# Kernel optimization log

Hardware: AMD Instinct MI355X
Metric: run time of the kernel (lower is better)

The kernel has to match this reference:

```python
import jax, jax.numpy as jnp
import numpy as np

D = 1024        # d_hidden
DE = 512        # d_expert (routed)
E = 8           # n_routed_experts
TOP_K = 2
DS = DE * 2     # shared expert width = d_expert * n_shared_experts


def setup_inputs() -> dict:
    key = jax.random.key(0)
    ks = jax.random.split(key, 8)
    s = 1.0 / np.sqrt(D)
    return {
        "x": jax.random.normal(ks[0], (2, 1024, D), dtype=jnp.float32),
        "W_g": jax.random.normal(ks[1], (D, E), dtype=jnp.float32) * s,
        "Wg_e": jax.random.normal(ks[2], (E, D, DE), dtype=jnp.float32) * s,
        "Wu_e": jax.random.normal(ks[3], (E, D, DE), dtype=jnp.float32) * s,
        "Wd_e": jax.random.normal(ks[4], (E, DE, D), dtype=jnp.float32) * (1.0 / np.sqrt(DE)),
        "Wg_s": jax.random.normal(ks[5], (D, DS), dtype=jnp.float32) * s,
        "Wu_s": jax.random.normal(ks[6], (D, DS), dtype=jnp.float32) * s,
        "Wd_s": jax.random.normal(ks[7], (DS, D), dtype=jnp.float32) * (1.0 / np.sqrt(DS)),
    }


def _moe(x, W_g, Wg_e, Wu_e, Wd_e, Wg_s, Wu_s, Wd_s):
    B, T, Dm = x.shape
    N = B * T
    xf = x.reshape(N, Dm)

    # shared expert (SwiGLU)
    shared = (jax.nn.silu(xf @ Wg_s) * (xf @ Wu_s)) @ Wd_s  # [N, D]

    # gating: softmax then top-k (set membership identical to torch sorted=False)
    probs = jax.nn.softmax(xf @ W_g, axis=-1)               # [N, E]
    topk_vals, topk_ids = jax.lax.top_k(probs, TOP_K)       # [N, K]

    # combine weights c[n, e] = sum of topk_vals where routed to expert e
    # (equivalent to the original gather -> weighted scatter_add combine)
    c = jnp.zeros((N, E), dtype=x.dtype)
    c = c.at[jnp.arange(N)[:, None], topk_ids].add(topk_vals)

    # dense per-expert SwiGLU, weighted-combined (same math as gather/scatter loop)
    gate = jax.nn.silu(jnp.einsum('nd,edh->neh', xf, Wg_e))
    up = jnp.einsum('nd,edh->neh', xf, Wu_e)
    routed = jnp.einsum('neh,ne,ehd->nd', gate * up, c, Wd_e)  # [N, D]

    return (shared + routed).reshape(B, T, Dm)


def reference(x, W_g, Wg_e, Wu_e, Wd_e, Wg_s, Wu_s, Wd_s):
    return _moe(x, W_g, Wg_e, Wu_e, Wd_e, Wg_s, Wu_s, Wd_s)
```

## Files before the change

### kernel.cpp

```cpp
#include <hip/hip_runtime.h>
#include <hip/hip_bf16.h>

#define NTOK 2048
#define DIM  1024
#define DEXP 512
#define NEXP 8
#define DSH  1024
#define KH   5120
#define MAXROWS 5120

typedef __hip_bfloat16 bf16;
typedef __attribute__((ext_vector_type(8))) short bf16x8;
typedef __attribute__((ext_vector_type(4))) float floatx4;

__device__ __forceinline__ void gl_lds16(const bf16* g, bf16* l) {
    __builtin_amdgcn_global_load_lds(
        (const __attribute__((address_space(1))) void*)g,
        (__attribute__((address_space(3))) void*)l, 16, 0, 0);
}

__device__ __forceinline__ float b2f(short s) {
    union { float f; unsigned u; } v;
    v.u = ((unsigned)(unsigned short)s) << 16;
    return v.f;
}

struct B4 { bf16 a, b, c, d; };

__global__ __launch_bounds__(256) void gate_logits(const float* __restrict__ x,
                                                   const float* __restrict__ Wg,
                                                   bf16* __restrict__ Xb,
                                                   int2* __restrict__ te,
                                                   float2* __restrict__ tp) {
    int t = blockIdx.x * 4 + (threadIdx.x >> 6);
    int lane = threadIdx.x & 63;
    const float* xr = x + (long)t * DIM;
    bf16* xo = Xb + (long)t * DIM;
    float acc[NEXP] = {0.f, 0.f, 0.f, 0.f, 0.f, 0.f, 0.f, 0.f};
#pragma unroll
    for (int i = 0; i < 4; i++) {
        int d = lane * 4 + i * 256;
        float4 xv = *(const float4*)(xr + d);
        B4 o{__float2bfloat16(xv.x), __float2bfloat16(xv.y),
             __float2bfloat16(xv.z), __float2bfloat16(xv.w)};
        *(B4*)(xo + d) = o;
#pragma unroll
        for (int j = 0; j < 4; j++) {
            float xs = (j == 0) ? xv.x : (j == 1) ? xv.y : (j == 2) ? xv.z : xv.w;
            float4 w0 = *(const float4*)(Wg + (d + j) * NEXP);
            float4 w1 = *(const float4*)(Wg + (d + j) * NEXP + 4);
            acc[0] += xs * w0.x; acc[1] += xs * w0.y; acc[2] += xs * w0.z; acc[3] += xs * w0.w;
            acc[4] += xs * w1.x; acc[5] += xs * w1.y; acc[6] += xs * w1.z; acc[7] += xs * w1.w;
        }
    }
#pragma unroll
    for (int e = 0; e < NEXP; e++)
#pragma unroll
        for (int off = 32; off; off >>= 1)
            acc[e] += __shfl_xor(acc[e], off);
    if (lane == 0) {
        float m = acc[0];
#pragma unroll
        for (int e = 1; e < NEXP; e++) m = fmaxf(m, acc[e]);
        float p[NEXP], s = 0.f;
#pragma unroll
        for (int e = 0; e < NEXP; e++) { p[e] = expf(acc[e] - m); s += p[e]; }
        float inv = 1.f / s;
#pragma unroll
        for (int e = 0; e < NEXP; e++) p[e] *= inv;
        int i1 = 0;
#pragma unroll
        for (int e = 1; e < NEXP; e++) if (p[e] > p[i1]) i1 = e;
        int i2 = (i1 == 0) ? 1 : 0;
#pragma unroll
        for (int e = 0; e < NEXP; e++) if (e != i1 && p[e] > p[i2]) i2 = e;
        te[t] = make_int2(i1, i2);
        tp[t] = make_float2(p[i1], p[i2]);
    }
}

__global__ __launch_bounds__(512) void assign_kernel(const int2* __restrict__ te,
                                                     const float2* __restrict__ tp,
                                                     int* __restrict__ counts,
                                                     int* __restrict__ offs,
                                                     int* __restrict__ tok_list,
                                                     float* __restrict__ cw,
                                                     int* __restrict__ s1a,
                                                     int* __restrict__ s2a) {
    __shared__ int cnt[NEXP];
    const int e = threadIdx.x >> 6;
    const int lane = threadIdx.x & 63;
    int base = 0;
    for (int t0 = 0; t0 < NTOK; t0 += 64) {
        int t = t0 + lane;
        int2 ee = te[t];
        bool m1 = (ee.x == e), m2 = (ee.y == e);
        bool mt = m1 || m2;
        unsigned long long mask = __ballot(mt);
        int pre = __popcll(mask & ((1ull << lane) - 1ull));
        if (mt) {
            int slot = base + pre;
            tok_list[e * NTOK + slot] = t;
            float2 pp = tp[t];
            cw[e * NTOK + slot] = m1 ? pp.x : pp.y;
            if (m1) s1a[t] = slot; else s2a[t] = slot;
        }
        base += __popcll(mask);
    }
    if (lane == 0) cnt[e] = base;
    __syncthreads();
    if (threadIdx.x == 0) {
        int o = 0;
#pragma unroll
        for (int i = 0; i < NEXP; i++) {
            counts[i] = cnt[i];
            offs[i] = o;
            o += (cnt[i] + 127) & ~127;
        }
    }
}

__global__ __launch_bounds__(256) void pack_weights(
        const float* __restrict__ Wg_s, const float* __restrict__ Wu_s,
        const float* __restrict__ Wg_e, const float* __restrict__ Wu_e,
        const float* __restrict__ Wd_s, const float* __restrict__ Wd_e,
        bf16* __restrict__ Bg, bf16* __restrict__ Bu, bf16* __restrict__ Bd) {
    __shared__ float t[32][36];
    int b = blockIdx.x;
    const float* src; bf16* dst; int C; long dstStride, dstBase; int tilesX;
    if (b < 1024)       { src = Wg_s; dst = Bg; C = 1024; dstStride = 1024; dstBase = 0; tilesX = 32; }
    else if (b < 2048)  { b -= 1024; src = Wu_s; dst = Bu; C = 1024; dstStride = 1024; dstBase = 0; tilesX = 32; }
    else if (b < 6144)  { b -= 2048; int z = b >> 9; b &= 511;
                          src = Wg_e + (long)z * DIM * DEXP; dst = Bg; C = 512;
                          dstStride = 1024; dstBase = (long)(DSH + z * DEXP) * 1024; tilesX = 16; }
    else if (b < 10240) { b -= 6144; int z = b >> 9; b &= 511;
                          src = Wu_e + (long)z * DIM * DEXP; dst = Bu; C = 512;
                          dstStride = 1024; dstBase = (long)(DSH + z * DEXP) * 1024; tilesX = 16; }
    else if (b < 11264) { b -= 10240; src = Wd_s; dst = Bd; C = 1024; dstStride = KH; dstBase = 0; tilesX = 32; }
    else                { b -= 11264; int z = b >> 9; b &= 511;
                          src = Wd_e + (long)z * DEXP * DIM; dst = Bd; C = 1024;
                          dstStride = KH; dstBase = DSH + (long)z * DEXP; tilesX = 32; }
    int tileX = b & (tilesX - 1), tileY = b / tilesX;
    int c0 = tileX * 32, r0 = tileY * 32;

    {
        int row = threadIdx.x >> 3, ch = threadIdx.x & 7;
        float4 v = *(const float4*)(src + (long)(r0 + row) * C + c0 + ch * 4);
        *(float4*)(&t[row][ch * 4]) = v;
    }
    __syncthreads();
    {
        int dc = threadIdx.x & 31, ch = threadIdx.x >> 5;
        int j = ch * 4;
        B4 o{__float2bfloat16(t[j][dc]), __float2bfloat16(t[j + 1][dc]),
             __float2bfloat16(t[j + 2][dc]), __float2bfloat16(t[j + 3][dc])};
        *(B4*)(dst + dstBase + (long)(c0 + dc) * dstStride + r0 + j) = o;
    }
}

__global__ __launch_bounds__(256) void gu_all(const bf16* __restrict__ X,
                                              const bf16* __restrict__ Bg,
                                              const bf16* __restrict__ Bu,
                                              const int* __restrict__ counts,
                                              const int* __restrict__ offs,
                                              const int* __restrict__ tok_list,
                                              const float* __restrict__ cw,
                                              bf16* __restrict__ Hs,
                                              bf16* __restrict__ He) {
    __shared__ __align__(16) bf16 sA[128 * 32];
    __shared__ __align__(16) bf16 sBg[64 * 32];
    __shared__ __align__(16) bf16 sBu[64 * 32];

    const int b = blockIdx.x;
    const bool routed = b < 1024;
    int e = 0, m, c;
    if (routed) {
        e = b >> 7; m = (b >> 3) & 15; c = b & 7;
        if (m * 128 >= counts[e]) return;
    } else {
        int bs = b - 1024; m = bs >> 4; c = bs & 15;
    }
    const int so = routed ? offs[e] : 0;
    const int colB0 = routed ? (DSH + e * DEXP + c * 64) : c * 64;

    const int tid = threadIdx.x;
    const int wave = tid >> 6, lane = tid & 63;
    const int wr = wave >> 1, wc = wave & 1;
    const int q = lane >> 4, l15 = lane & 15;
    const int koff = (q ^ ((l15 >> 1) & 3)) * 8;

    const int r0 = tid >> 2, c4 = tid & 3;
    const int r1 = r0 + 64;
    const int c4s = c4 ^ ((r0 >> 1) & 3);
    long aRow0, aRow1;
    if (routed) {
        const int* tl = tok_list + e * NTOK + m * 128;
        aRow0 = (long)tl[r0] * DIM;
        aRow1 = (long)tl[r1] * DIM;
    } else {
        aRow0 = (long)(m * 128 + r0) * DIM;
        aRow1 = (long)(m * 128 + r1) * DIM;
    }
    const long bRow = (long)(colB0 + r0) * DIM;

    floatx4 accG[4][2], accU[4][2];
    const floatx4 z4 = {0.f, 0.f, 0.f, 0.f};
#pragma unroll
    for (int i = 0; i < 4; i++)
#pragma unroll
        for (int j = 0; j < 2; j++) { accG[i][j] = z4; accU[i][j] = z4; }

    for (int k0 = 0; k0 < DIM; k0 += 32) {
        gl_lds16(X + aRow0 + k0 + c4s * 8, sA + (wave * 64) * 8);
        gl_lds16(X + aRow1 + k0 + c4s * 8, sA + (256 + wave * 64) * 8);
        gl_lds16(Bg + bRow + k0 + c4s * 8, sBg + (wave * 64) * 8);
        gl_lds16(Bu + bRow + k0 + c4s * 8, sBu + (wave * 64) * 8);
        __syncthreads();

        bf16x8 af[4], bg[2], bu[2];
#pragma unroll
        for (int rt = 0; rt < 4; rt++)
            af[rt] = *(const bf16x8*)(sA + (wr * 64 + rt * 16 + l15) * 32 + koff);
#pragma unroll
        for (int ct = 0; ct < 2; ct++) {
            int cb = (wc * 32 + ct * 16 + l15) * 32 + koff;
            bg[ct] = *(const bf16x8*)(sBg + cb);
            bu[ct] = *(const bf16x8*)(sBu + cb);
        }
#pragma unroll
        for (int rt = 0; rt < 4; rt++)
#pragma unroll
            for (int ct = 0; ct < 2; ct++) {
                accG[rt][ct] = __builtin_amdgcn_mfma_f32_16x16x32_bf16(af[rt], bg[ct], accG[rt][ct], 0, 0, 0);
                accU[rt][ct] = __builtin_amdgcn_mfma_f32_16x16x32_bf16(af[rt], bu[ct], accU[rt][ct], 0, 0, 0);
            }
        __syncthreads();
    }

    float wv[4][4];
#pragma unroll
    for (int rt = 0; rt < 4; rt++)
#pragma unroll
        for (int r = 0; r < 4; r++) {
            int srow = wr * 64 + rt * 16 + q * 4 + r;
            wv[rt][r] = routed ? cw[e * NTOK + m * 128 + srow] : 1.0f;
        }
#pragma unroll
    for (int rt = 0; rt < 4; rt++)
#pragma unroll
        for (int ct = 0; ct < 2; ct++)
#pragma unroll
            for (int r = 0; r < 4; r++) {
                int srow = wr * 64 + rt * 16 + q * 4 + r;
                int colLoc = c * 64 + wc * 32 + ct * 16 + l15;
                float g = accG[rt][ct][r];
                float u = accU[rt][ct][r];
                float h = (g / (1.f + __expf(-g))) * u * wv[rt][r];
                if (routed)
                    He[(long)(so + m * 128 + srow) * DEXP + colLoc] = __float2bfloat16(h);
                else
                    Hs[(long)(m * 128 + srow) * DSH + colLoc] = __float2bfloat16(h);
            }
}

__global__ __launch_bounds__(256) void down_all(const bf16* __restrict__ Hs,
                                                const bf16* __restrict__ He,
                                                const bf16* __restrict__ Bd,
                                                const int* __restrict__ counts,
                                                const int* __restrict__ offs,
                                                bf16* __restrict__ Ys,
                                                bf16* __restrict__ Ye) {
    __shared__ __align__(16) bf16 sA[128 * 32];
    __shared__ __align__(16) bf16 sB[64 * 32];

    const int b = blockIdx.x;
    const bool routed = b < 2048;
    int e = 0, m, cc;
    if (routed) {
        e = b >> 8; m = (b >> 4) & 15; cc = b & 15;
        if (m * 128 >= counts[e]) return;
    } else {
        int bs = b - 2048; m = bs >> 4; cc = bs & 15;
    }
    const int so = routed ? offs[e] : 0;
    const bf16* A = routed ? He + (long)so * DEXP : Hs;
    bf16* Y = routed ? Ye + (long)so * DIM : Ys;
    const int astr = routed ? DEXP : DSH;
    const int ksteps = routed ? (DEXP / 32) : (DSH / 32);
    const int kg0 = routed ? (DSH + e * DEXP) : 0;

    const int tid = threadIdx.x;
    const int wave = tid >> 6, lane = tid & 63;
    const int wr = wave >> 1, wc = wave & 1;
    const int q = lane >> 4, l15 = lane & 15;
    const int koff = (q ^ ((l15 >> 1) & 3)) * 8;

    const int r0 = tid >> 2, c4 = tid & 3;
    const int r1 = r0 + 64;
    const int c4s = c4 ^ ((r0 >> 1) & 3);
    const long aRow0 = (long)(m * 128 + r0) * astr;
    const long aRow1 = (long)(m * 128 + r1) * astr;
    const long bRow = (long)(cc * 64 + r0) * KH + kg0;

    floatx4 acc[4][2];
    const floatx4 z4 = {0.f, 0.f, 0.f, 0.f};
#pragma unroll
    for (int i = 0; i < 4; i++)
#pragma unroll
        for (int j = 0; j < 2; j++) acc[i][j] = z4;

    for (int ks = 0; ks < ksteps; ks++) {
        const int k0 = ks * 32;
        gl_lds16(A + aRow0 + k0 + c4s * 8, sA + (wave * 64) * 8);
        gl_lds16(A + aRow1 + k0 + c4s * 8, sA + (256 + wave * 64) * 8);
        gl_lds16(Bd + bRow + k0 + c4s * 8, sB + (wave * 64) * 8);
        __syncthreads();

        bf16x8 af[4], bb[2];
#pragma unroll
        for (int rt = 0; rt < 4; rt++)
            af[rt] = *(const bf16x8*)(sA + (wr * 64 + rt * 16 + l15) * 32 + koff);
#pragma unroll
        for (int ct = 0; ct < 2; ct++)
            bb[ct] = *(const bf16x8*)(sB + (wc * 32 + ct * 16 + l15) * 32 + koff);
#pragma unroll
        for (int rt = 0; rt < 4; rt++)
#pragma unroll
            for (int ct = 0; ct < 2; ct++)
                acc[rt][ct] = __builtin_amdgcn_mfma_f32_16x16x32_bf16(af[rt], bb[ct], acc[rt][ct], 0, 0, 0);
        __syncthreads();
    }

#pragma unroll
    for (int rt = 0; rt < 4; rt++)
#pragma unroll
        for (int ct = 0; ct < 2; ct++)
#pragma unroll
            for (int r = 0; r < 4; r++) {
                int srow = wr * 64 + rt * 16 + q * 4 + r;
                int mc = cc * 64 + wc * 32 + ct * 16 + l15;
                Y[(long)(m * 128 + srow) * DIM + mc] = __float2bfloat16(acc[rt][ct][r]);
            }
}

__global__ __launch_bounds__(256) void combine_kernel(const bf16* __restrict__ Ys,
                                                      const bf16* __restrict__ Ye,
                                                      const int2* __restrict__ te,
                                                      const int* __restrict__ s1a,
                                                      const int* __restrict__ s2a,
                                                      const int* __restrict__ offs,
                                                      float* __restrict__ out) {
    int idx = blockIdx.x * 256 + threadIdx.x;
    int t = idx >> 7;
    int d = (idx & 127) * 8;
    int2 ee = te[t];
    long r1 = (long)(offs[ee.x] + s1a[t]);
    long r2 = (long)(offs[ee.y] + s2a[t]);
    bf16x8 a = *(const bf16x8*)(Ys + (long)t * DIM + d);
    bf16x8 p = *(const bf16x8*)(Ye + r1 * DIM + d);
    bf16x8 r = *(const bf16x8*)(Ye + r2 * DIM + d);
    float* o = out + (long)t * DIM + d;
#pragma unroll
    for (int i = 0; i < 8; i++)
        o[i] = b2f(a[i]) + b2f(p[i]) + b2f(r[i]);
}

extern "C" void kernel_launch(void* const* d_in, const int* in_sizes, int n_in,
                              void* d_out, int out_size, void* d_ws, size_t ws_size,
                              hipStream_t stream) {
    const float* x    = (const float*)d_in[0];
    const float* W_g  = (const float*)d_in[1];
    const float* Wg_e = (const float*)d_in[2];
    const float* Wu_e = (const float*)d_in[3];
    const float* Wd_e = (const float*)d_in[4];
    const float* Wg_s = (const float*)d_in[5];
    const float* Wu_s = (const float*)d_in[6];
    const float* Wd_s = (const float*)d_in[7];
    float* out = (float*)d_out;

    bf16* Xb = (bf16*)d_ws;
    bf16* Bg = Xb + (size_t)NTOK * DIM;
    bf16* Bu = Bg + (size_t)KH * DIM;
    bf16* Bd = Bu + (size_t)KH * DIM;
    bf16* Hs = Bd + (size_t)DIM * KH;
    bf16* He = Hs + (size_t)NTOK * DSH;
    bf16* Ys = He + (size_t)MAXROWS * DEXP;
    bf16* Ye = Ys + (size_t)NTOK * DIM;
    int*  counts   = (int*)(Ye + (size_t)MAXROWS * DIM);
    int*  offs     = counts + NEXP;
    int*  tok_list = offs + NEXP;
    float* cw      = (float*)(tok_list + NEXP * NTOK);
    int*  s1a      = (int*)(cw + NEXP * NTOK);
    int*  s2a      = s1a + NTOK;
    int2* te       = (int2*)(s2a + NTOK);
    float2* tp     = (float2*)(te + NTOK);

    hipMemsetAsync(tok_list, 0,
                   sizeof(int) * NEXP * NTOK + sizeof(float) * NEXP * NTOK, stream);
    gate_logits<<<NTOK / 4, 256, 0, stream>>>(x, W_g, Xb, te, tp);
    assign_kernel<<<1, 512, 0, stream>>>(te, tp, counts, offs, tok_list, cw, s1a, s2a);
    pack_weights<<<15360, 256, 0, stream>>>(Wg_s, Wu_s, Wg_e, Wu_e, Wd_s, Wd_e, Bg, Bu, Bd);
    gu_all<<<1280, 256, 0, stream>>>(Xb, Bg, Bu, counts, offs, tok_list, cw, Hs, He);
    down_all<<<2304, 256, 0, stream>>>(Hs, He, Bd, counts, offs, Ys, Ye);
    combine_kernel<<<NTOK * DIM / 8 / 256, 256, 0, stream>>>(Ys, Ye, te, s1a, s2a, offs, out);
}
```

Measured before the change: 208.5 us.

## Fuse gating with weight packing, drop memset, widen down-proj tiles

```diff
diff --git a/kernel.cpp b/kernel.cpp
--- a/kernel.cpp
+++ b/kernel.cpp
@@ -27,55 +27,90 @@
 
 struct B4 { bf16 a, b, c, d; };
 
-__global__ __launch_bounds__(256) void gate_logits(const float* __restrict__ x,
-                                                   const float* __restrict__ Wg,
-                                                   bf16* __restrict__ Xb,
-                                                   int2* __restrict__ te,
-                                                   float2* __restrict__ tp) {
-    int t = blockIdx.x * 4 + (threadIdx.x >> 6);
-    int lane = threadIdx.x & 63;
-    const float* xr = x + (long)t * DIM;
-    bf16* xo = Xb + (long)t * DIM;
-    float acc[NEXP] = {0.f, 0.f, 0.f, 0.f, 0.f, 0.f, 0.f, 0.f};
-#pragma unroll
-    for (int i = 0; i < 4; i++) {
-        int d = lane * 4 + i * 256;
-        float4 xv = *(const float4*)(xr + d);
-        B4 o{__float2bfloat16(xv.x), __float2bfloat16(xv.y),
-             __float2bfloat16(xv.z), __float2bfloat16(xv.w)};
-        *(B4*)(xo + d) = o;
-#pragma unroll
-        for (int j = 0; j < 4; j++) {
-            float xs = (j == 0) ? xv.x : (j == 1) ? xv.y : (j == 2) ? xv.z : xv.w;
-            float4 w0 = *(const float4*)(Wg + (d + j) * NEXP);
-            float4 w1 = *(const float4*)(Wg + (d + j) * NEXP + 4);
-            acc[0] += xs * w0.x; acc[1] += xs * w0.y; acc[2] += xs * w0.z; acc[3] += xs * w0.w;
-            acc[4] += xs * w1.x; acc[5] += xs * w1.y; acc[6] += xs * w1.z; acc[7] += xs * w1.w;
-        }
-    }
-#pragma unroll
-    for (int e = 0; e < NEXP; e++)
-#pragma unroll
-        for (int off = 32; off; off >>= 1)
-            acc[e] += __shfl_xor(acc[e], off);
-    if (lane == 0) {
-        float m = acc[0];
-#pragma unroll
-        for (int e = 1; e < NEXP; e++) m = fmaxf(m, acc[e]);
-        float p[NEXP], s = 0.f;
-#pragma unroll
-        for (int e = 0; e < NEXP; e++) { p[e] = expf(acc[e] - m); s += p[e]; }
-        float inv = 1.f / s;
-#pragma unroll
-        for (int e = 0; e < NEXP; e++) p[e] *= inv;
-        int i1 = 0;
-#pragma unroll
-        for (int e = 1; e < NEXP; e++) if (p[e] > p[i1]) i1 = e;
-        int i2 = (i1 == 0) ? 1 : 0;
-#pragma unroll
-        for (int e = 0; e < NEXP; e++) if (e != i1 && p[e] > p[i2]) i2 = e;
-        te[t] = make_int2(i1, i2);
-        tp[t] = make_float2(p[i1], p[i2]);
+__global__ __launch_bounds__(256) void prep_kernel(
+        const float* __restrict__ x, const float* __restrict__ Wg,
+        const float* __restrict__ Wg_s, const float* __restrict__ Wu_s,
+        const float* __restrict__ Wg_e, const float* __restrict__ Wu_e,
+        const float* __restrict__ Wd_s, const float* __restrict__ Wd_e,
+        bf16* __restrict__ Xb, int2* __restrict__ te, float2* __restrict__ tp,
+        bf16* __restrict__ Bg, bf16* __restrict__ Bu, bf16* __restrict__ Bd) {
+    __shared__ float t[32][36];
+    if (blockIdx.x < 512) {
+        int tok = blockIdx.x * 4 + (threadIdx.x >> 6);
+        int lane = threadIdx.x & 63;
+        const float* xr = x + (long)tok * DIM;
+        bf16* xo = Xb + (long)tok * DIM;
+        float acc[NEXP] = {0.f, 0.f, 0.f, 0.f, 0.f, 0.f, 0.f, 0.f};
+#pragma unroll
+        for (int i = 0; i < 4; i++) {
+            int d = lane * 4 + i * 256;
+            float4 xv = *(const float4*)(xr + d);
+            B4 o{__float2bfloat16(xv.x), __float2bfloat16(xv.y),
+                 __float2bfloat16(xv.z), __float2bfloat16(xv.w)};
+            *(B4*)(xo + d) = o;
+#pragma unroll
+            for (int j = 0; j < 4; j++) {
+                float xs = (j == 0) ? xv.x : (j == 1) ? xv.y : (j == 2) ? xv.z : xv.w;
+                float4 w0 = *(const float4*)(Wg + (d + j) * NEXP);
+                float4 w1 = *(const float4*)(Wg + (d + j) * NEXP + 4);
+                acc[0] += xs * w0.x; acc[1] += xs * w0.y; acc[2] += xs * w0.z; acc[3] += xs * w0.w;
+                acc[4] += xs * w1.x; acc[5] += xs * w1.y; acc[6] += xs * w1.z; acc[7] += xs * w1.w;
+            }
+        }
+#pragma unroll
+        for (int e = 0; e < NEXP; e++)
+#pragma unroll
+            for (int off = 32; off; off >>= 1)
+                acc[e] += __shfl_xor(acc[e], off);
+        if (lane == 0) {
+            float m = acc[0];
+#pragma unroll
+            for (int e = 1; e < NEXP; e++) m = fmaxf(m, acc[e]);
+            float p[NEXP], s = 0.f;
+#pragma unroll
+            for (int e = 0; e < NEXP; e++) { p[e] = expf(acc[e] - m); s += p[e]; }
+            float inv = 1.f / s;
+#pragma unroll
+            for (int e = 0; e < NEXP; e++) p[e] *= inv;
+            int i1 = 0;
+#pragma unroll
+            for (int e = 1; e < NEXP; e++) if (p[e] > p[i1]) i1 = e;
+            int i2 = (i1 == 0) ? 1 : 0;
+#pragma unroll
+            for (int e = 0; e < NEXP; e++) if (e != i1 && p[e] > p[i2]) i2 = e;
+            te[tok] = make_int2(i1, i2);
+            tp[tok] = make_float2(p[i1], p[i2]);
+        }
+        return;
+    }
+    int b = blockIdx.x - 512;
+    const float* src; bf16* dst; int C; long dstStride, dstBase; int tilesX;
+    if (b < 1024)       { src = Wg_s; dst = Bg; C = 1024; dstStride = 1024; dstBase = 0; tilesX = 32; }
+    else if (b < 2048)  { b -= 1024; src = Wu_s; dst = Bu; C = 1024; dstStride = 1024; dstBase = 0; tilesX = 32; }
+    else if (b < 6144)  { b -= 2048; int z = b >> 9; b &= 511;
+                          src = Wg_e + (long)z * DIM * DEXP; dst = Bg; C = 512;
+                          dstStride = 1024; dstBase = (long)(DSH + z * DEXP) * 1024; tilesX = 16; }
+    else if (b < 10240) { b -= 6144; int z = b >> 9; b &= 511;
+                          src = Wu_e + (long)z * DIM * DEXP; dst = Bu; C = 512;
+                          dstStride = 1024; dstBase = (long)(DSH + z * DEXP) * 1024; tilesX = 16; }
+    else if (b < 11264) { b -= 10240; src = Wd_s; dst = Bd; C = 1024; dstStride = KH; dstBase = 0; tilesX = 32; }
+    else                { b -= 11264; int z = b >> 9; b &= 511;
+                          src = Wd_e + (long)z * DEXP * DIM; dst = Bd; C = 1024;
+                          dstStride = KH; dstBase = DSH + (long)z * DEXP; tilesX = 32; }
+    int tileX = b & (tilesX - 1), tileY = b / tilesX;
+    int c0 = tileX * 32, tr0 = tileY * 32;
+    {
+        int row = threadIdx.x >> 3, ch = threadIdx.x & 7;
+        float4 v = *(const float4*)(src + (long)(tr0 + row) * C + c0 + ch * 4);
+        *(float4*)(&t[row][ch * 4]) = v;
+    }
+    __syncthreads();
+    {
+        int dc = threadIdx.x & 31, ch = threadIdx.x >> 5;
+        int j = ch * 4;
+        B4 o{__float2bfloat16(t[j][dc]), __float2bfloat16(t[j + 1][dc]),
+             __float2bfloat16(t[j + 2][dc]), __float2bfloat16(t[j + 3][dc])};
+        *(B4*)(dst + dstBase + (long)(c0 + dc) * dstStride + tr0 + j) = o;
     }
 }
 
@@ -107,6 +142,11 @@
         }
         base += __popcll(mask);
     }
+    int rc = (base + 127) & ~127;
+    for (int s = base + lane; s < rc; s += 64) {
+        tok_list[e * NTOK + s] = 0;
+        cw[e * NTOK + s] = 0.f;
+    }
     if (lane == 0) cnt[e] = base;
     __syncthreads();
     if (threadIdx.x == 0) {
@@ -120,53 +160,15 @@
     }
 }
 
-__global__ __launch_bounds__(256) void pack_weights(
-        const float* __restrict__ Wg_s, const float* __restrict__ Wu_s,
-        const float* __restrict__ Wg_e, const float* __restrict__ Wu_e,
-        const float* __restrict__ Wd_s, const float* __restrict__ Wd_e,
-        bf16* __restrict__ Bg, bf16* __restrict__ Bu, bf16* __restrict__ Bd) {
-    __shared__ float t[32][36];
-    int b = blockIdx.x;
-    const float* src; bf16* dst; int C; long dstStride, dstBase; int tilesX;
-    if (b < 1024)       { src = Wg_s; dst = Bg; C = 1024; dstStride = 1024; dstBase = 0; tilesX = 32; }
-    else if (b < 2048)  { b -= 1024; src = Wu_s; dst = Bu; C = 1024; dstStride = 1024; dstBase = 0; tilesX = 32; }
-    else if (b < 6144)  { b -= 2048; int z = b >> 9; b &= 511;
-                          src = Wg_e + (long)z * DIM * DEXP; dst = Bg; C = 512;
-                          dstStride = 1024; dstBase = (long)(DSH + z * DEXP) * 1024; tilesX = 16; }
-    else if (b < 10240) { b -= 6144; int z = b >> 9; b &= 511;
-                          src = Wu_e + (long)z * DIM * DEXP; dst = Bu; C = 512;
-                          dstStride = 1024; dstBase = (long)(DSH + z * DEXP) * 1024; tilesX = 16; }
-    else if (b < 11264) { b -= 10240; src = Wd_s; dst = Bd; C = 1024; dstStride = KH; dstBase = 0; tilesX = 32; }
-    else                { b -= 11264; int z = b >> 9; b &= 511;
-                          src = Wd_e + (long)z * DEXP * DIM; dst = Bd; C = 1024;
-                          dstStride = KH; dstBase = DSH + (long)z * DEXP; tilesX = 32; }
-    int tileX = b & (tilesX - 1), tileY = b / tilesX;
-    int c0 = tileX * 32, r0 = tileY * 32;
-
-    {
-        int row = threadIdx.x >> 3, ch = threadIdx.x & 7;
-        float4 v = *(const float4*)(src + (long)(r0 + row) * C + c0 + ch * 4);
-        *(float4*)(&t[row][ch * 4]) = v;
-    }
-    __syncthreads();
-    {
-        int dc = threadIdx.x & 31, ch = threadIdx.x >> 5;
-        int j = ch * 4;
-        B4 o{__float2bfloat16(t[j][dc]), __float2bfloat16(t[j + 1][dc]),
-             __float2bfloat16(t[j + 2][dc]), __float2bfloat16(t[j + 3][dc])};
-        *(B4*)(dst + dstBase + (long)(c0 + dc) * dstStride + r0 + j) = o;
-    }
-}
-
-__global__ __launch_bounds__(256) void gu_all(const bf16* __restrict__ X,
-                                              const bf16* __restrict__ Bg,
-                                              const bf16* __restrict__ Bu,
-                                              const int* __restrict__ counts,
-                                              const int* __restrict__ offs,
-                                              const int* __restrict__ tok_list,
-                                              const float* __restrict__ cw,
-                                              bf16* __restrict__ Hs,
-                                              bf16* __restrict__ He) {
+__global__ __launch_bounds__(256) void gu_kernel(const bf16* __restrict__ X,
+                                                 const bf16* __restrict__ Bg,
+                                                 const bf16* __restrict__ Bu,
+                                                 const int* __restrict__ counts,
+                                                 const int* __restrict__ offs,
+                                                 const int* __restrict__ tok_list,
+                                                 const float* __restrict__ cw,
+                                                 bf16* __restrict__ Hs,
+                                                 bf16* __restrict__ He) {
     __shared__ __align__(16) bf16 sA[128 * 32];
     __shared__ __align__(16) bf16 sBg[64 * 32];
     __shared__ __align__(16) bf16 sBu[64 * 32];
@@ -188,7 +190,6 @@
     const int wr = wave >> 1, wc = wave & 1;
     const int q = lane >> 4, l15 = lane & 15;
     const int koff = (q ^ ((l15 >> 1) & 3)) * 8;
-
     const int r0 = tid >> 2, c4 = tid & 3;
     const int r1 = r0 + 64;
     const int c4s = c4 ^ ((r0 >> 1) & 3);
@@ -263,24 +264,24 @@
             }
 }
 
-__global__ __launch_bounds__(256) void down_all(const bf16* __restrict__ Hs,
-                                                const bf16* __restrict__ He,
-                                                const bf16* __restrict__ Bd,
-                                                const int* __restrict__ counts,
-                                                const int* __restrict__ offs,
-                                                bf16* __restrict__ Ys,
-                                                bf16* __restrict__ Ye) {
+__global__ __launch_bounds__(256) void down_kernel(const bf16* __restrict__ Hs,
+                                                   const bf16* __restrict__ He,
+                                                   const bf16* __restrict__ Bd,
+                                                   const int* __restrict__ counts,
+                                                   const int* __restrict__ offs,
+                                                   bf16* __restrict__ Ys,
+                                                   bf16* __restrict__ Ye) {
     __shared__ __align__(16) bf16 sA[128 * 32];
-    __shared__ __align__(16) bf16 sB[64 * 32];
+    __shared__ __align__(16) bf16 sB[128 * 32];
 
     const int b = blockIdx.x;
-    const bool routed = b < 2048;
+    const bool routed = b < 1024;
     int e = 0, m, cc;
     if (routed) {
-        e = b >> 8; m = (b >> 4) & 15; cc = b & 15;
+        e = b >> 7; int rem = b & 127; m = rem >> 3; cc = rem & 7;
         if (m * 128 >= counts[e]) return;
     } else {
-        int bs = b - 2048; m = bs >> 4; cc = bs & 15;
+        int bs = b - 1024; m = bs >> 3; cc = bs & 7;
     }
     const int so = routed ? offs[e] : 0;
     const bf16* A = routed ? He + (long)so * DEXP : Hs;
@@ -294,39 +295,40 @@
     const int wr = wave >> 1, wc = wave & 1;
     const int q = lane >> 4, l15 = lane & 15;
     const int koff = (q ^ ((l15 >> 1) & 3)) * 8;
-
     const int r0 = tid >> 2, c4 = tid & 3;
     const int r1 = r0 + 64;
     const int c4s = c4 ^ ((r0 >> 1) & 3);
     const long aRow0 = (long)(m * 128 + r0) * astr;
     const long aRow1 = (long)(m * 128 + r1) * astr;
-    const long bRow = (long)(cc * 64 + r0) * KH + kg0;
-
-    floatx4 acc[4][2];
+    const long bRow0 = (long)(cc * 128 + r0) * KH + kg0;
+    const long bRow1 = (long)(cc * 128 + r1) * KH + kg0;
+
+    floatx4 acc[4][4];
     const floatx4 z4 = {0.f, 0.f, 0.f, 0.f};
 #pragma unroll
     for (int i = 0; i < 4; i++)
 #pragma unroll
-        for (int j = 0; j < 2; j++) acc[i][j] = z4;
+        for (int j = 0; j < 4; j++) acc[i][j] = z4;
 
     for (int ks = 0; ks < ksteps; ks++) {
         const int k0 = ks * 32;
         gl_lds16(A + aRow0 + k0 + c4s * 8, sA + (wave * 64) * 8);
         gl_lds16(A + aRow1 + k0 + c4s * 8, sA + (256 + wave * 64) * 8);
-        gl_lds16(Bd + bRow + k0 + c4s * 8, sB + (wave * 64) * 8);
+        gl_lds16(Bd + bRow0 + k0 + c4s * 8, sB + (wave * 64) * 8);
+        gl_lds16(Bd + bRow1 + k0 + c4s * 8, sB + (256 + wave * 64) * 8);
         __syncthreads();
 
-        bf16x8 af[4], bb[2];
+        bf16x8 af[4], bb[4];
 #pragma unroll
         for (int rt = 0; rt < 4; rt++)
             af[rt] = *(const bf16x8*)(sA + (wr * 64 + rt * 16 + l15) * 32 + koff);
 #pragma unroll
-        for (int ct = 0; ct < 2; ct++)
-            bb[ct] = *(const bf16x8*)(sB + (wc * 32 + ct * 16 + l15) * 32 + koff);
+        for (int ct = 0; ct < 4; ct++)
+            bb[ct] = *(const bf16x8*)(sB + (wc * 64 + ct * 16 + l15) * 32 + koff);
 #pragma unroll
         for (int rt = 0; rt < 4; rt++)
 #pragma unroll
-            for (int ct = 0; ct < 2; ct++)
+            for (int ct = 0; ct < 4; ct++)
                 acc[rt][ct] = __builtin_amdgcn_mfma_f32_16x16x32_bf16(af[rt], bb[ct], acc[rt][ct], 0, 0, 0);
         __syncthreads();
     }
@@ -334,11 +336,11 @@
 #pragma unroll
     for (int rt = 0; rt < 4; rt++)
 #pragma unroll
-        for (int ct = 0; ct < 2; ct++)
+        for (int ct = 0; ct < 4; ct++)
 #pragma unroll
             for (int r = 0; r < 4; r++) {
                 int srow = wr * 64 + rt * 16 + q * 4 + r;
-                int mc = cc * 64 + wc * 32 + ct * 16 + l15;
+                int mc = cc * 128 + wc * 64 + ct * 16 + l15;
                 Y[(long)(m * 128 + srow) * DIM + mc] = __float2bfloat16(acc[rt][ct][r]);
             }
 }
@@ -354,11 +356,11 @@
     int t = idx >> 7;
     int d = (idx & 127) * 8;
     int2 ee = te[t];
-    long r1 = (long)(offs[ee.x] + s1a[t]);
-    long r2 = (long)(offs[ee.y] + s2a[t]);
+    long rr1 = (long)(offs[ee.x] + s1a[t]);
+    long rr2 = (long)(offs[ee.y] + s2a[t]);
     bf16x8 a = *(const bf16x8*)(Ys + (long)t * DIM + d);
-    bf16x8 p = *(const bf16x8*)(Ye + r1 * DIM + d);
-    bf16x8 r = *(const bf16x8*)(Ye + r2 * DIM + d);
+    bf16x8 p = *(const bf16x8*)(Ye + rr1 * DIM + d);
+    bf16x8 r = *(const bf16x8*)(Ye + rr2 * DIM + d);
     float* o = out + (long)t * DIM + d;
 #pragma unroll
     for (int i = 0; i < 8; i++)
@@ -395,12 +397,10 @@
     int2* te       = (int2*)(s2a + NTOK);
     float2* tp     = (float2*)(te + NTOK);
 
-    hipMemsetAsync(tok_list, 0,
-                   sizeof(int) * NEXP * NTOK + sizeof(float) * NEXP * NTOK, stream);
-    gate_logits<<<NTOK / 4, 256, 0, stream>>>(x, W_g, Xb, te, tp);
+    prep_kernel<<<512 + 15360, 256, 0, stream>>>(x, W_g, Wg_s, Wu_s, Wg_e, Wu_e,
+                                                 Wd_s, Wd_e, Xb, te, tp, Bg, Bu, Bd);
     assign_kernel<<<1, 512, 0, stream>>>(te, tp, counts, offs, tok_list, cw, s1a, s2a);
-    pack_weights<<<15360, 256, 0, stream>>>(Wg_s, Wu_s, Wg_e, Wu_e, Wd_s, Wd_e, Bg, Bu, Bd);
-    gu_all<<<1280, 256, 0, stream>>>(Xb, Bg, Bu, counts, offs, tok_list, cw, Hs, He);
-    down_all<<<2304, 256, 0, stream>>>(Hs, He, Bd, counts, offs, Ys, Ye);
+    gu_kernel<<<1280, 256, 0, stream>>>(Xb, Bg, Bu, counts, offs, tok_list, cw, Hs, He);
+    down_kernel<<<1152, 256, 0, stream>>>(Hs, He, Bd, counts, offs, Ys, Ye);
     combine_kernel<<<NTOK * DIM / 8 / 256, 256, 0, stream>>>(Ys, Ye, te, s1a, s2a, offs, out);
 }
```

New measurement: 212.1 us. No clear change (+1.7%).
